# Performance work log

Hardware: AMD Instinct MI355X
Metric: run time of the kernel (lower is better)

Reference implementation:

```python
import jax, jax.numpy as jnp
import numpy as np

COUPLE_STRENGTH = 0.1
ITER_FISTA = 16
ITER_EIGENVAL = 20


def setup_inputs() -> dict:
    key = jax.random.key(0)
    k1, k2 = jax.random.split(key)
    # light field patches: (b, N, u, v, s, t, ch)
    x = jax.random.normal(k1, (8, 256, 5, 5, 4, 4, 3), dtype=jnp.float32)
    dim_signal = 5 * 5 * 4 * 4 * 3  # 1200
    dim_dict = 2 * dim_signal       # overcompleteness = 2 -> 2400
    D = jax.random.normal(k2, (dim_signal, dim_dict), dtype=jnp.float32)
    D = D / jnp.linalg.norm(D, axis=0, keepdims=True)  # UnitNorm(axis=0) constraint
    return {"x": x, "dictionary": D}


def _max_eigval(D):
    """von Mises power iteration for largest eigenvalue of D^T D."""
    v0 = jax.random.normal(jax.random.key(42), (D.shape[1],), dtype=D.dtype)
    v0 = v0 / jnp.linalg.norm(v0)

    def step(v, _):
        w = D.T @ (D @ v)
        n = jnp.linalg.norm(w)
        return w / n, n

    _, norms = jax.lax.scan(step, v0, None, length=ITER_EIGENVAL)
    return norms[-1]


def _soft_threshold(x, thr):
    return jnp.sign(x) * jnp.maximum(jnp.abs(x) - thr, 0.0)


def _sparse_code_fista(x2, D):
    """x2: (B, N, dim_signal); D: (dim_signal, dim_dict) -> codes (B, N, dim_dict)."""
    L = _max_eigval(D)            # Lipschitz constant of grad of 0.5*||Dz - x||^2
    thr = COUPLE_STRENGTH / L
    z0 = jnp.zeros(x2.shape[:-1] + (D.shape[1],), dtype=x2.dtype)
    carry0 = (z0, z0, jnp.float32(1.0))  # (z, y, t)

    def step(carry, _):
        z, y, t = carry
        recon = jnp.einsum('bnk,dk->bnd', y, D)             # (B,N,ds)
        grad = jnp.einsum('bnd,dk->bnk', recon - x2, D)     # (B,N,dd)
        z_new = _soft_threshold(y - grad / L, thr)
        t_new = 0.5 * (1.0 + jnp.sqrt(1.0 + 4.0 * t * t))
        y_new = z_new + ((t - 1.0) / t_new) * (z_new - z)   # Nesterov momentum
        return (z_new, y_new, t_new), None

    (z, _, _), _ = jax.lax.scan(step, carry0, None, length=ITER_FISTA)
    return z


def reference(x, dictionary):
    B, N, u, v, s, t, ch = x.shape
    x2 = x.reshape(B, N, u * v * s * t * ch)
    code = jax.lax.stop_gradient(_sparse_code_fista(x2, dictionary))
    recon = jnp.einsum('bnk,dk->bnd', code, dictionary)  # matmul(x, D, transpose_b=True)
    return recon.reshape(B, N, u, v, s, t, ch)
```

## Files before the change

kernel.cpp:

```cpp
#include <hip/hip_runtime.h>
#include <hip/hip_bf16.h>
#include <cmath>

#define DS 1200
#define DD 2400
#define MR 2048
#define KP 1216
#define NP1 1280
#define NG 2432
#define PPI 150

typedef __attribute__((ext_vector_type(8))) short s16x8;
typedef __attribute__((ext_vector_type(4))) float f32x4;

__device__ __forceinline__ float s2f(short s) {
    union { unsigned u; float f; } c;
    c.u = ((unsigned)(unsigned short)s) << 16;
    return c.f;
}
__device__ __forceinline__ short f2s(float f) {
    __hip_bfloat16 h = __float2bfloat16(f);
    return *reinterpret_cast<short*>(&h);
}


__device__ __forceinline__ unsigned rotl32(unsigned x, int d) {
    return (x << d) | (x >> (32 - d));
}

__device__ void threefry2x32(unsigned k0, unsigned k1, unsigned x0, unsigned x1,
                             unsigned* o0, unsigned* o1) {
    unsigned ks0 = k0, ks1 = k1, ks2 = k0 ^ k1 ^ 0x1BD11BDAu;
    const int rotA[4] = {13, 15, 26, 6};
    const int rotB[4] = {17, 29, 16, 24};
    x0 += ks0; x1 += ks1;
    #pragma unroll
    for (int r = 0; r < 4; r++) { x0 += x1; x1 = rotl32(x1, rotA[r]); x1 ^= x0; }
    x0 += ks1; x1 += ks2 + 1u;
    #pragma unroll
    for (int r = 0; r < 4; r++) { x0 += x1; x1 = rotl32(x1, rotB[r]); x1 ^= x0; }
    x0 += ks2; x1 += ks0 + 2u;
    #pragma unroll
    for (int r = 0; r < 4; r++) { x0 += x1; x1 = rotl32(x1, rotA[r]); x1 ^= x0; }
    x0 += ks0; x1 += ks1 + 3u;
    #pragma unroll
    for (int r = 0; r < 4; r++) { x0 += x1; x1 = rotl32(x1, rotB[r]); x1 ^= x0; }
    x0 += ks1; x1 += ks2 + 4u;
    #pragma unroll
    for (int r = 0; r < 4; r++) { x0 += x1; x1 = rotl32(x1, rotA[r]); x1 ^= x0; }
    x0 += ks2; x1 += ks0 + 5u;
    *o0 = x0; *o1 = x1;
}

__device__ float erfinv_f32(float x) {
    float w = -logf((1.0f - x) * (1.0f + x));
    float p;
    if (w < 5.0f) {
        w -= 2.5f;
        p = 2.81022636e-08f;
        p = fmaf(p, w, 3.43273939e-07f);
        p = fmaf(p, w, -3.5233877e-06f);
        p = fmaf(p, w, -4.39150654e-06f);
        p = fmaf(p, w, 0.00021858087f);
        p = fmaf(p, w, -0.00125372503f);
        p = fmaf(p, w, -0.00417768164f);
        p = fmaf(p, w, 0.246640727f);
        p = fmaf(p, w, 1.50140941f);
    } else {
        w = sqrtf(w) - 3.0f;
        p = -0.000200214257f;
        p = fmaf(p, w, 0.000100950558f);
        p = fmaf(p, w, 0.00134934322f);
        p = fmaf(p, w, -0.00367342844f);
        p = fmaf(p, w, 0.00573950773f);
        p = fmaf(p, w, -0.0076224613f);
        p = fmaf(p, w, 0.00943887047f);
        p = fmaf(p, w, 1.00167406f);
        p = fmaf(p, w, 2.83297682f);
    }
    return p * x;
}

__device__ float bits_to_normal(unsigned bits) {
    unsigned fb = (bits >> 9) | 0x3F800000u;
    float u01 = __uint_as_float(fb) - 1.0f;
    const float lo = -0.99999994f;
    float u = u01 * 2.0f + lo;
    u = fmaxf(lo, u);
    return 1.41421356237f * erfinv_f32(u);
}

__global__ void k_init(float* __restrict__ w0, float* __restrict__ w1,
                       float* __restrict__ part) {
    int tid = threadIdx.x;
    for (int i = tid; i < 21 * PPI; i += 256) part[i] = 0.0f;
    if (tid < 32) {
        w0[2400 + tid] = 0.0f;
        w1[2400 + tid] = 0.0f;
    }
    __shared__ float red[256];
    float local2 = 0.0f;
    for (int p = tid; p < DS; p += 256) {
        unsigned r0, r1;
        threefry2x32(0u, 42u, (unsigned)p, (unsigned)(DS + p), &r0, &r1);
        float n0 = bits_to_normal(r0);
        float n1 = bits_to_normal(r1);
        w0[p] = n0;
        w0[DS + p] = n1;
        local2 += n0 * n0 + n1 * n1;
    }
    red[tid] = local2;
    __syncthreads();
    for (int s = 128; s > 0; s >>= 1) {
        if (tid < s) red[tid] += red[tid + s];
        __syncthreads();
    }
    if (tid == 0) part[0] = red[0];
}

__global__ __launch_bounds__(1024) void k_gmv(const short* __restrict__ Grm,
                                              const float* __restrict__ win,
                                              const float* __restrict__ partin,
                                              float* __restrict__ wout,
                                              float* __restrict__ partout) {
    float s2 = 0.0f;
    for (int i = 0; i < PPI; i++) s2 += partin[i];
    float rn = 1.0f / sqrtf(s2);
    int wave = threadIdx.x >> 6, lane = threadIdx.x & 63;
    int row = blockIdx.x * 16 + wave;
    const s16x8* gh = (const s16x8*)(Grm + (size_t)row * NG);
    const float4* w4 = (const float4*)win;
    float acc = 0.0f;
    #pragma unroll
    for (int i = 0; i < 5; i++) {
        int c = lane + i * 64;
        if (c < 304) {
            s16x8 h = gh[c];
            float4 wa = w4[c * 2], wb = w4[c * 2 + 1];
            acc += s2f(h[0]) * wa.x + s2f(h[1]) * wa.y;
            acc += s2f(h[2]) * wa.z + s2f(h[3]) * wa.w;
            acc += s2f(h[4]) * wb.x + s2f(h[5]) * wb.y;
            acc += s2f(h[6]) * wb.z + s2f(h[7]) * wb.w;
        }
    }
    #pragma unroll
    for (int off = 32; off > 0; off >>= 1) acc += __shfl_xor(acc, off, 64);
    __shared__ float red[16];
    if (lane == 0) {
        float val = acc * rn;
        wout[row] = val;
        red[wave] = val * val;
    }
    __syncthreads();
    if (threadIdx.x == 0) {
        float s = 0.0f;
        #pragma unroll
        for (int i = 0; i < 16; i++) s += red[i];
        partout[blockIdx.x] = s;
    }
}

__global__ void k_fin(const float* __restrict__ part20, float* __restrict__ scal) {
    if (threadIdx.x == 0) {
        float s = 0.0f;
        for (int i = 0; i < PPI; i++) s += part20[i];
        float L = sqrtf(s);
        scal[0] = L;
        scal[1] = 1.0f / L;
        scal[2] = 0.1f / L;
    }
}

__global__ void k_makeD(const float* __restrict__ D, short* __restrict__ Dp) {
    int p = blockIdx.x * 256 + threadIdx.x;
    if (p >= NP1 * NG) return;
    int tile = p >> 10, win = p & 1023;
    int row = win >> 3, e = win & 7;
    int mt = tile / (NG >> 3), ct = tile % (NG >> 3);
    int d = mt * 128 + row, n = ct * 8 + e;
    float v = (d < DS && n < DD) ? D[(size_t)d * DD + n] : 0.0f;
    Dp[p] = f2s(v);
}

__global__ void k_makeX(const float* __restrict__ x,
                        short* __restrict__ Xhi, short* __restrict__ Xlo) {
    int p = blockIdx.x * 256 + threadIdx.x;
    if (p >= MR * KP) return;
    int tile = p >> 10, win = p & 1023;
    int row = win >> 3, e = win & 7;
    int mt = tile / (KP >> 3), ct = tile % (KP >> 3);
    int m = mt * 128 + row, k = ct * 8 + e;
    float v = (k < DS) ? x[(size_t)m * DS + k] : 0.0f;
    short h = f2s(v);
    Xhi[p] = h;
    Xlo[p] = f2s(v - s2f(h));
}

__global__ void k_makeDt(const float* __restrict__ D,
                         short* __restrict__ Dthi, short* __restrict__ Dtlo) {
    __shared__ float t[32][33];
    int bc = blockIdx.x * 32;
    int bk = blockIdx.y * 32;
    int tx = threadIdx.x & 31, ty = threadIdx.x >> 5;
    for (int i = ty; i < 32; i += 8) {
        int k = bk + i, c = bc + tx;
        t[i][tx] = (k < DS && c < DD) ? D[(size_t)k * DD + c] : 0.0f;
    }
    __syncthreads();
    for (int i = ty; i < 32; i += 8) {
        int c = bc + i, k = bk + tx;
        float v = t[tx][i];
        short h = f2s(v);
        size_t po = ((size_t)(c >> 7) * (KP >> 3) + (k >> 3)) * 1024 +
                    ((c & 127) << 3) + (k & 7);
        Dthi[po] = h;
        Dtlo[po] = f2s(v - s2f(h));
    }
}

__global__ void k_makeW(const float* __restrict__ Gf, const float* __restrict__ scal,
                        short* __restrict__ Wp) {
    int i = blockIdx.x * 256 + threadIdx.x;
    if (i >= NG * NG / 8) return;
    float invL = scal[1];
    int e0 = i * 8;
    int band = e0 / (128 * NG);
    int rem = e0 - band * (128 * NG);
    int tile = rem >> 10;
    int row = (rem & 1023) >> 3;
    int m = band * 128 + row;
    int k0 = tile * 8;
    const float4* gp = (const float4*)(Gf + (size_t)m * NG + k0);
    float4 g0 = gp[0], g1 = gp[1];
    float gv[8] = {g0.x, g0.y, g0.z, g0.w, g1.x, g1.y, g1.z, g1.w};
    s16x8 wv;
    #pragma unroll
    for (int e = 0; e < 8; e++) {
        float wf = ((k0 + e == m) ? 1.0f : 0.0f) - gv[e] * invL;
        wv[e] = f2s(wf);
    }
    ((s16x8*)Wp)[i] = wv;
}

__global__ void k_fista0(const short* __restrict__ XDL, const float* __restrict__ scal,
                         short* __restrict__ Z, short* __restrict__ Y) {
    int i = blockIdx.x * 256 + threadIdx.x;
    if (i >= MR * NG / 8) return;
    float thr = scal[2];
    s16x8 xv = ((const s16x8*)XDL)[i];
    s16x8 zs;
    #pragma unroll
    for (int k = 0; k < 8; k++) {
        float gs = s2f(xv[k]);
        float az = fabsf(gs) - thr;
        float zn = (az > 0.0f) ? copysignf(az, gs) : 0.0f;
        zs[k] = f2s(zn);
    }
    ((s16x8*)Z)[i] = zs;
    ((s16x8*)Y)[i] = zs;
}

__device__ __forceinline__ void gload16(const void* g, void* l) {
    __builtin_amdgcn_global_load_lds(
        (const __attribute__((address_space(1))) unsigned int*)g,
        (__attribute__((address_space(3))) unsigned int*)l, 16, 0, 0);
}

template <int EPI, bool SPLIT>
__global__ __launch_bounds__(256, 2) void mfma_gemm(
    const short* __restrict__ Ah, const short* __restrict__ Al, int CA,
    const short* __restrict__ Bh, const short* __restrict__ Bl, int CB,
    int K, int swz,
    const short* __restrict__ XDLp, const float* __restrict__ scal, float mom,
    short* __restrict__ Ynew, short* __restrict__ Zst,
    short* __restrict__ Grm,
    float* __restrict__ Out) {
    constexpr int ALO = 2048;
    constexpr int BHO = 4096;
    constexpr int BLO = 8192;
    constexpr int BUF = 12288;
    __shared__ __align__(16) short lds[3 * BUF];

    const int tid = threadIdx.x;
    const int w = tid >> 6, lane = tid & 63;
    const int fm = lane & 15, kg = lane >> 4;
    const int wr = w >> 1, wc = w & 1;

    int bx, by;
    if (swz) {
        int q = gridDim.x >> 3;
        int s = (blockIdx.x & 7) * q + (blockIdx.x >> 3);
        by = s & 31; bx = s >> 5;
    } else { bx = blockIdx.x; by = blockIdx.y; }
    const int m0 = by * 64, n0 = bx * 128;

    f32x4 acc[2][4];
    #pragma unroll
    for (int g = 0; g < 2; ++g)
        #pragma unroll
        for (int h = 0; h < 4; ++h) acc[g][h] = f32x4{0.f, 0.f, 0.f, 0.f};

    float invL = 0.0f, thr = 0.0f;
    if (EPI == 2) thr = scal[2];
    if (EPI == 3) invL = scal[1];

    const int half = (m0 >> 6) & 1;
    const int nk = K / (SPLIT ? 32 : 64);

    const size_t AbS = (size_t)(m0 & ~127) * CA + w * 1024 + half * 512 + lane * 8;
    const size_t BbS = (size_t)n0 * CB + w * 512 + lane * 8;
    const size_t AbN = (size_t)(m0 & ~127) * CA + half * 512 + lane * 8;
    const size_t BbN = (size_t)n0 * CB + lane * 8;

    auto STAGE = [&](int t, int cur) {
        short* bp = &lds[cur * BUF];
        if constexpr (SPLIT) {
            const size_t kk = (size_t)t << 12;
            gload16(Ah + AbS + kk, bp + w * 512);
            gload16(Bh + BbS + kk, bp + BHO + w * 512);
            gload16(Bh + BbS + kk + 2048, bp + BHO + 2048 + w * 512);
            gload16(Al + AbS + kk, bp + ALO + w * 512);
            gload16(Bl + BbS + kk, bp + BLO + w * 512);
            gload16(Bl + BbS + kk + 2048, bp + BLO + 2048 + w * 512);
        } else {
            const size_t kk = (size_t)t << 13;
            const int cs0 = 2 * w, cs1 = 2 * w + 1;
            gload16(Ah + AbN + kk + cs0 * 1024, bp + cs0 * 512);
            gload16(Ah + AbN + kk + cs1 * 1024, bp + cs1 * 512);
            gload16(Bh + BbN + kk + cs0 * 1024,       bp + BHO + cs0 * 1024);
            gload16(Bh + BbN + kk + cs0 * 1024 + 512, bp + BHO + cs0 * 1024 + 512);
            gload16(Bh + BbN + kk + cs1 * 1024,       bp + BHO + cs1 * 1024);
            gload16(Bh + BbN + kk + cs1 * 1024 + 512, bp + BHO + cs1 * 1024 + 512);
        }
    };

    STAGE(0, 0);
    STAGE(1, 1);

    int rb = 0, sb = 2;
    for (int t = 0; t < nk; ++t) {
        if (t < nk - 1)
            asm volatile("s_waitcnt vmcnt(6)" ::: "memory");
        else
            asm volatile("s_waitcnt vmcnt(0)" ::: "memory");
        __builtin_amdgcn_s_barrier();
        asm volatile("" ::: "memory");
        if (t + 2 < nk) STAGE(t + 2, sb);
        const short* bs = &lds[rb * BUF];

        #pragma unroll
        for (int ks = 0; ks < (SPLIT ? 1 : 2); ++ks) {
            const int c = ks * 4 + kg;
            s16x8 a[2], b[4];
            #pragma unroll
            for (int g = 0; g < 2; ++g)
                a[g] = *(const s16x8*)&bs[c * 512 + (wr * 32 + g * 16 + fm) * 8];
            #pragma unroll
            for (int h = 0; h < 4; ++h)
                b[h] = *(const s16x8*)&bs[BHO + c * 1024 + (wc * 64 + h * 16 + fm) * 8];
            if constexpr (SPLIT) {
                s16x8 a2[2], b2[4];
                #pragma unroll
                for (int g = 0; g < 2; ++g)
                    a2[g] = *(const s16x8*)&bs[ALO + c * 512 + (wr * 32 + g * 16 + fm) * 8];
                #pragma unroll
                for (int h = 0; h < 4; ++h)
                    b2[h] = *(const s16x8*)&bs[BLO + c * 1024 + (wc * 64 + h * 16 + fm) * 8];
                #pragma unroll
                for (int g = 0; g < 2; ++g)
                    #pragma unroll
                    for (int h = 0; h < 4; ++h) {
                        acc[g][h] = __builtin_amdgcn_mfma_f32_16x16x32_bf16(a[g], b[h], acc[g][h], 0, 0, 0);
                        acc[g][h] = __builtin_amdgcn_mfma_f32_16x16x32_bf16(a[g], b2[h], acc[g][h], 0, 0, 0);
                        acc[g][h] = __builtin_amdgcn_mfma_f32_16x16x32_bf16(a2[g], b[h], acc[g][h], 0, 0, 0);
                    }
            } else {
                #pragma unroll
                for (int g = 0; g < 2; ++g)
                    #pragma unroll
                    for (int h = 0; h < 4; ++h)
                        acc[g][h] = __builtin_amdgcn_mfma_f32_16x16x32_bf16(a[g], b[h], acc[g][h], 0, 0, 0);
            }
        }
        rb = (rb == 2) ? 0 : rb + 1;
        sb = (sb == 2) ? 0 : sb + 1;
    }

    #pragma unroll
    for (int g = 0; g < 2; ++g) {
        #pragma unroll
        for (int h = 0; h < 4; ++h) {
            #pragma unroll
            for (int j = 0; j < 4; ++j) {
                int m = m0 + wr * 32 + g * 16 + kg * 4 + j;
                int n = n0 + wc * 64 + h * 16 + fm;
                float v = acc[g][h][j];
                if (EPI == 0) {
                    if (n < DS) Out[(size_t)m * DS + n] = v;
                } else if (EPI == 2) {
                    size_t pz = (size_t)(m & ~127) * NG + ((n >> 3) << 10) +
                                ((m & 127) << 3) + (n & 7);
                    float gs = v + s2f(XDLp[pz]);
                    float az = fabsf(gs) - thr;
                    float zn = (az > 0.0f) ? copysignf(az, gs) : 0.0f;
                    float zold = s2f(Zst[pz]);
                    float yn = zn + mom * (zn - zold);
                    Zst[pz] = f2s(zn);
                    Ynew[pz] = f2s(yn);
                } else if (EPI == 3) {
                    size_t pz = (size_t)(m & ~127) * NG + ((n >> 3) << 10) +
                                ((m & 127) << 3) + (n & 7);
                    Ynew[pz] = f2s(v * invL);
                } else {
                    size_t o = (size_t)m * NG + n;
                    Grm[o] = f2s(v);
                    Out[o] = v;
                }
            }
        }
    }
}

extern "C" void kernel_launch(void* const* d_in, const int* in_sizes, int n_in,
                              void* d_out, int out_size, void* d_ws, size_t ws_size,
                              hipStream_t stream) {
    const float* x = (const float*)d_in[0];
    const float* D = (const float*)d_in[1];
    float* out = (float*)d_out;

    char* wsb = (char*)d_ws;
    float* w0 = (float*)wsb;
    float* w1 = w0 + 2432;
    float* part = w1 + 2432;
    float* scal = part + 3200;

    char* p = wsb + 65536;
    short* Dp   = (short*)p; p += (size_t)NP1 * NG * 2;
    short* Dthi = (short*)p; p += (size_t)NG * KP * 2;
    short* Dtlo = (short*)p; p += (size_t)NG * KP * 2;
    short* Xhi  = (short*)p; p += (size_t)MR * KP * 2;
    short* Xlo  = (short*)p; p += (size_t)MR * KP * 2;
    short* Wp   = (short*)p; p += (size_t)NG * NG * 2;
    short* Grm  = (short*)p; p += (size_t)NG * NG * 2;
    short* XDLp = (short*)p; p += (size_t)MR * NG * 2;
    short* Ya   = (short*)p; p += (size_t)MR * NG * 2;
    short* Yb   = (short*)p; p += (size_t)MR * NG * 2;
    short* Zp   = (short*)p; p += (size_t)MR * NG * 2;
    float* Gf   = (float*)Ya;

    k_makeD<<<(NP1 * NG + 255) / 256, 256, 0, stream>>>(D, Dp);
    k_makeDt<<<dim3(NG / 32, KP / 32), 256, 0, stream>>>(D, Dthi, Dtlo);
    k_makeX<<<(MR * KP + 255) / 256, 256, 0, stream>>>(x, Xhi, Xlo);

    mfma_gemm<4, true><<<dim3(NG / 128, NG / 64), 256, 0, stream>>>(
        Dthi, Dtlo, KP, Dthi, Dtlo, KP, KP, 0,
        nullptr, nullptr, 0.0f, nullptr, nullptr, Grm, Gf);

    k_init<<<1, 256, 0, stream>>>(w0, w1, part);
    for (int j = 0; j < 20; j++) {
        const float* win = (j & 1) ? w1 : w0;
        float* wout = (j & 1) ? w0 : w1;
        k_gmv<<<PPI, 1024, 0, stream>>>(Grm, win, part + j * PPI, wout,
                                        part + (j + 1) * PPI);
    }
    k_fin<<<1, 64, 0, stream>>>(part + 20 * PPI, scal);

    k_makeW<<<(NG * NG / 8 + 255) / 256, 256, 0, stream>>>(Gf, scal, Wp);

    mfma_gemm<3, true><<<dim3(608), 256, 0, stream>>>(
        Xhi, Xlo, KP, Dthi, Dtlo, KP, KP, 1,
        nullptr, scal, 0.0f, XDLp, nullptr, nullptr, nullptr);

    k_fista0<<<(MR * NG / 8 + 255) / 256, 256, 0, stream>>>(XDLp, scal, Zp, Ya);

    float t = 1.6180339887f;
    for (int i = 1; i < 16; i++) {
        float tn = 0.5f * (1.0f + sqrtf(1.0f + 4.0f * t * t));
        float mom = (t - 1.0f) / tn;
        t = tn;
        short* Yc = (i & 1) ? Ya : Yb;
        short* Yn = (i & 1) ? Yb : Ya;
        mfma_gemm<2, false><<<dim3(608), 256, 0, stream>>>(
            Yc, nullptr, NG, Wp, nullptr, NG, NG, 1,
            XDLp, scal, mom, Yn, Zp, nullptr, nullptr);
    }

    mfma_gemm<0, false><<<dim3(320), 256, 0, stream>>>(
        Zp, nullptr, NG, Dp, nullptr, NG, NG, 1,
        nullptr, nullptr, 0.0f, nullptr, nullptr, nullptr, out);
}
```

Baseline: 1.002 ms.

## Add dedicated FISTA GEMM loading A from global into registers, double-buffer B

Adds a specialized fista_gemm kernel for the 15 FISTA iterations. It loads the Y operand directly from global memory into registers, stages only the W operand through a two-slot LDS buffer, and lowers LDS use so three blocks fit per CU. The generic mfma_gemm drops from a triple-buffered, vmcnt-tuned pipeline to plain double buffering with __syncthreads, raises its launch bound to 4 blocks, and gets a new block swizzle. The intent is more occupancy and less LDS traffic in the hot loop, at the risk of exposed global-load latency on the A operand and shallower prefetch in the other GEMMs.

```diff
diff --git a/kernel.cpp b/kernel.cpp
--- a/kernel.cpp
+++ b/kernel.cpp
@@ -266,20 +266,147 @@
         (__attribute__((address_space(3))) unsigned int*)l, 16, 0, 0);
 }
 
+__global__ __launch_bounds__(256, 3) void fista_gemm(
+    const short* __restrict__ Yp, const short* __restrict__ Wq,
+    const short* __restrict__ XDLp, const float* __restrict__ scal, float mom,
+    short* __restrict__ Ynew, short* __restrict__ Zst) {
+    __shared__ __align__(16) short ldsB[2][8192];
+
+    const int tid = threadIdx.x;
+    const int w = tid >> 6, lane = tid & 63;
+    const int fm = lane & 15, kg = lane >> 4;
+    const int wr = w >> 1, wc = w & 1;
+
+    const int b = blockIdx.x;
+    const int sv = b >> 3;
+    const int bx = sv >> 2;
+    const int by = (b & 7) * 4 + (sv & 3);
+    const int m0 = by * 64, n0 = bx * 128;
+
+    f32x4 acc[2][4];
+    #pragma unroll
+    for (int g = 0; g < 2; ++g)
+        #pragma unroll
+        for (int h = 0; h < 4; ++h) acc[g][h] = f32x4{0.f, 0.f, 0.f, 0.f};
+
+    const float thr = scal[2];
+
+    const int band = m0 & ~127, half = (m0 >> 6) & 1;
+    const short* Abase = Yp + (size_t)band * NG +
+                         (half * 64 + wr * 32 + fm) * 8 + kg * 1024;
+    const short* Bbase = Wq + (size_t)n0 * NG + tid * 8;
+
+    s16x8 aA0, aA1, aA2, aA3, aB0, aB1, aB2, aB3;
+
+#define LOADA(st, r0, r1, r2, r3)                         \
+    {                                                     \
+        const short* p_ = Abase + (size_t)(st) * 8192;    \
+        r0 = *(const s16x8*)(p_);                         \
+        r1 = *(const s16x8*)(p_ + 128);                   \
+        r2 = *(const s16x8*)(p_ + 4096);                  \
+        r3 = *(const s16x8*)(p_ + 4224);                  \
+    }
+#define STAGEB(st, buf)                                   \
+    {                                                     \
+        const short* q_ = Bbase + (size_t)(st) * 8192;    \
+        short* bp_ = &ldsB[buf][0];                       \
+        gload16(q_, bp_ + w * 512);                       \
+        gload16(q_ + 2048, bp_ + 2048 + w * 512);         \
+        gload16(q_ + 4096, bp_ + 4096 + w * 512);         \
+        gload16(q_ + 6144, bp_ + 6144 + w * 512);         \
+    }
+#define COMP(buf, r0, r1, r2, r3)                                              \
+    {                                                                          \
+        const short* bs_ = &ldsB[buf][0];                                      \
+        {                                                                      \
+            const int c_ = kg;                                                 \
+            s16x8 b0 = *(const s16x8*)&bs_[c_ * 1024 + (wc * 64 + 0 * 16 + fm) * 8];  \
+            s16x8 b1 = *(const s16x8*)&bs_[c_ * 1024 + (wc * 64 + 1 * 16 + fm) * 8];  \
+            s16x8 b2 = *(const s16x8*)&bs_[c_ * 1024 + (wc * 64 + 2 * 16 + fm) * 8];  \
+            s16x8 b3 = *(const s16x8*)&bs_[c_ * 1024 + (wc * 64 + 3 * 16 + fm) * 8];  \
+            acc[0][0] = __builtin_amdgcn_mfma_f32_16x16x32_bf16(r0, b0, acc[0][0], 0, 0, 0); \
+            acc[0][1] = __builtin_amdgcn_mfma_f32_16x16x32_bf16(r0, b1, acc[0][1], 0, 0, 0); \
+            acc[0][2] = __builtin_amdgcn_mfma_f32_16x16x32_bf16(r0, b2, acc[0][2], 0, 0, 0); \
+            acc[0][3] = __builtin_amdgcn_mfma_f32_16x16x32_bf16(r0, b3, acc[0][3], 0, 0, 0); \
+            acc[1][0] = __builtin_amdgcn_mfma_f32_16x16x32_bf16(r1, b0, acc[1][0], 0, 0, 0); \
+            acc[1][1] = __builtin_amdgcn_mfma_f32_16x16x32_bf16(r1, b1, acc[1][1], 0, 0, 0); \
+            acc[1][2] = __builtin_amdgcn_mfma_f32_16x16x32_bf16(r1, b2, acc[1][2], 0, 0, 0); \
+            acc[1][3] = __builtin_amdgcn_mfma_f32_16x16x32_bf16(r1, b3, acc[1][3], 0, 0, 0); \
+        }                                                                      \
+        {                                                                      \
+            const int c_ = 4 + kg;                                             \
+            s16x8 b0 = *(const s16x8*)&bs_[c_ * 1024 + (wc * 64 + 0 * 16 + fm) * 8];  \
+            s16x8 b1 = *(const s16x8*)&bs_[c_ * 1024 + (wc * 64 + 1 * 16 + fm) * 8];  \
+            s16x8 b2 = *(const s16x8*)&bs_[c_ * 1024 + (wc * 64 + 2 * 16 + fm) * 8];  \
+            s16x8 b3 = *(const s16x8*)&bs_[c_ * 1024 + (wc * 64 + 3 * 16 + fm) * 8];  \
+            acc[0][0] = __builtin_amdgcn_mfma_f32_16x16x32_bf16(r2, b0, acc[0][0], 0, 0, 0); \
+            acc[0][1] = __builtin_amdgcn_mfma_f32_16x16x32_bf16(r2, b1, acc[0][1], 0, 0, 0); \
+            acc[0][2] = __builtin_amdgcn_mfma_f32_16x16x32_bf16(r2, b2, acc[0][2], 0, 0, 0); \
+            acc[0][3] = __builtin_amdgcn_mfma_f32_16x16x32_bf16(r2, b3, acc[0][3], 0, 0, 0); \
+            acc[1][0] = __builtin_amdgcn_mfma_f32_16x16x32_bf16(r3, b0, acc[1][0], 0, 0, 0); \
+            acc[1][1] = __builtin_amdgcn_mfma_f32_16x16x32_bf16(r3, b1, acc[1][1], 0, 0, 0); \
+            acc[1][2] = __builtin_amdgcn_mfma_f32_16x16x32_bf16(r3, b2, acc[1][2], 0, 0, 0); \
+            acc[1][3] = __builtin_amdgcn_mfma_f32_16x16x32_bf16(r3, b3, acc[1][3], 0, 0, 0); \
+        }                                                                      \
+    }
+
+    LOADA(0, aA0, aA1, aA2, aA3);
+    STAGEB(0, 0);
+
+    for (int t = 0; t < 38; t += 2) {
+        __syncthreads();
+        STAGEB(t + 1, 1);
+        LOADA(t + 1, aB0, aB1, aB2, aB3);
+        COMP(0, aA0, aA1, aA2, aA3);
+        __syncthreads();
+        if (t + 2 < 38) {
+            STAGEB(t + 2, 0);
+            LOADA(t + 2, aA0, aA1, aA2, aA3);
+        }
+        COMP(1, aB0, aB1, aB2, aB3);
+    }
+
+#undef LOADA
+#undef STAGEB
+#undef COMP
+
+    #pragma unroll
+    for (int g = 0; g < 2; ++g) {
+        #pragma unroll
+        for (int h = 0; h < 4; ++h) {
+            #pragma unroll
+            for (int j = 0; j < 4; ++j) {
+                int m = m0 + wr * 32 + g * 16 + kg * 4 + j;
+                int n = n0 + wc * 64 + h * 16 + fm;
+                float v = acc[g][h][j];
+                size_t pz = (size_t)(m & ~127) * NG + ((n >> 3) << 10) +
+                            ((m & 127) << 3) + (n & 7);
+                float gs = v + s2f(XDLp[pz]);
+                float az = fabsf(gs) - thr;
+                float zn = (az > 0.0f) ? copysignf(az, gs) : 0.0f;
+                float zold = s2f(Zst[pz]);
+                float yn = zn + mom * (zn - zold);
+                Zst[pz] = f2s(zn);
+                Ynew[pz] = f2s(yn);
+            }
+        }
+    }
+}
+
 template <int EPI, bool SPLIT>
-__global__ __launch_bounds__(256, 2) void mfma_gemm(
+__global__ __launch_bounds__(256, 4) void mfma_gemm(
     const short* __restrict__ Ah, const short* __restrict__ Al, int CA,
     const short* __restrict__ Bh, const short* __restrict__ Bl, int CB,
     int K, int swz,
-    const short* __restrict__ XDLp, const float* __restrict__ scal, float mom,
-    short* __restrict__ Ynew, short* __restrict__ Zst,
+    const float* __restrict__ scal,
+    short* __restrict__ Ynew,
     short* __restrict__ Grm,
     float* __restrict__ Out) {
     constexpr int ALO = 2048;
     constexpr int BHO = 4096;
     constexpr int BLO = 8192;
     constexpr int BUF = 12288;
-    __shared__ __align__(16) short lds[3 * BUF];
+    __shared__ __align__(16) short lds[2 * BUF];
 
     const int tid = threadIdx.x;
     const int w = tid >> 6, lane = tid & 63;
@@ -288,9 +415,9 @@
 
     int bx, by;
     if (swz) {
-        int q = gridDim.x >> 3;
-        int s = (blockIdx.x & 7) * q + (blockIdx.x >> 3);
-        by = s & 31; bx = s >> 5;
+        int sv = blockIdx.x >> 3;
+        bx = sv >> 2;
+        by = (blockIdx.x & 7) * 4 + (sv & 3);
     } else { bx = blockIdx.x; by = blockIdx.y; }
     const int m0 = by * 64, n0 = bx * 128;
 
@@ -300,8 +427,7 @@
         #pragma unroll
         for (int h = 0; h < 4; ++h) acc[g][h] = f32x4{0.f, 0.f, 0.f, 0.f};
 
-    float invL = 0.0f, thr = 0.0f;
-    if (EPI == 2) thr = scal[2];
+    float invL = 0.0f;
     if (EPI == 3) invL = scal[1];
 
     const int half = (m0 >> 6) & 1;
@@ -335,18 +461,11 @@
     };
 
     STAGE(0, 0);
-    STAGE(1, 1);
-
-    int rb = 0, sb = 2;
+
     for (int t = 0; t < nk; ++t) {
-        if (t < nk - 1)
-            asm volatile("s_waitcnt vmcnt(6)" ::: "memory");
-        else
-            asm volatile("s_waitcnt vmcnt(0)" ::: "memory");
-        __builtin_amdgcn_s_barrier();
-        asm volatile("" ::: "memory");
-        if (t + 2 < nk) STAGE(t + 2, sb);
-        const short* bs = &lds[rb * BUF];
+        __syncthreads();
+        if (t + 1 < nk) STAGE(t + 1, (t + 1) & 1);
+        const short* bs = &lds[(t & 1) * BUF];
 
         #pragma unroll
         for (int ks = 0; ks < (SPLIT ? 1 : 2); ++ks) {
@@ -382,8 +501,6 @@
                         acc[g][h] = __builtin_amdgcn_mfma_f32_16x16x32_bf16(a[g], b[h], acc[g][h], 0, 0, 0);
             }
         }
-        rb = (rb == 2) ? 0 : rb + 1;
-        sb = (sb == 2) ? 0 : sb + 1;
     }
 
     #pragma unroll
@@ -397,16 +514,6 @@
                 float v = acc[g][h][j];
                 if (EPI == 0) {
                     if (n < DS) Out[(size_t)m * DS + n] = v;
-                } else if (EPI == 2) {
-                    size_t pz = (size_t)(m & ~127) * NG + ((n >> 3) << 10) +
-                                ((m & 127) << 3) + (n & 7);
-                    float gs = v + s2f(XDLp[pz]);
-                    float az = fabsf(gs) - thr;
-                    float zn = (az > 0.0f) ? copysignf(az, gs) : 0.0f;
-                    float zold = s2f(Zst[pz]);
-                    float yn = zn + mom * (zn - zold);
-                    Zst[pz] = f2s(zn);
-                    Ynew[pz] = f2s(yn);
                 } else if (EPI == 3) {
                     size_t pz = (size_t)(m & ~127) * NG + ((n >> 3) << 10) +
                                 ((m & 127) << 3) + (n & 7);
@@ -454,7 +561,7 @@
 
     mfma_gemm<4, true><<<dim3(NG / 128, NG / 64), 256, 0, stream>>>(
         Dthi, Dtlo, KP, Dthi, Dtlo, KP, KP, 0,
-        nullptr, nullptr, 0.0f, nullptr, nullptr, Grm, Gf);
+        nullptr, nullptr, Grm, Gf);
 
     k_init<<<1, 256, 0, stream>>>(w0, w1, part);
     for (int j = 0; j < 20; j++) {
@@ -469,7 +576,7 @@
 
     mfma_gemm<3, true><<<dim3(608), 256, 0, stream>>>(
         Xhi, Xlo, KP, Dthi, Dtlo, KP, KP, 1,
-        nullptr, scal, 0.0f, XDLp, nullptr, nullptr, nullptr);
+        scal, XDLp, nullptr, nullptr);
 
     k_fista0<<<(MR * NG / 8 + 255) / 256, 256, 0, stream>>>(XDLp, scal, Zp, Ya);
 
@@ -480,12 +587,11 @@
         t = tn;
         short* Yc = (i & 1) ? Ya : Yb;
         short* Yn = (i & 1) ? Yb : Ya;
-        mfma_gemm<2, false><<<dim3(608), 256, 0, stream>>>(
-            Yc, nullptr, NG, Wp, nullptr, NG, NG, 1,
-            XDLp, scal, mom, Yn, Zp, nullptr, nullptr);
+        fista_gemm<<<dim3(608), 256, 0, stream>>>(
+            Yc, Wp, XDLp, scal, mom, Yn, Zp);
     }
 
     mfma_gemm<0, false><<<dim3(320), 256, 0, stream>>>(
         Zp, nullptr, NG, Dp, nullptr, NG, NG, 1,
-        nullptr, nullptr, 0.0f, nullptr, nullptr, nullptr, out);
-}
+        nullptr, nullptr, nullptr, out);
+}
```

Result: slower. 1.028 ms (+2.5%).
